# Optimization experiments

Hardware: AMD Instinct MI355X
Metric: run time of the kernel (lower is better)

The kernel has to match this reference:

```python
import jax, jax.numpy as jnp
import numpy as np

# Mamba2 hyperparams (mamba_ssm defaults given __init__ args)
D_MODEL = 512
FF = 2048
D_STATE = 128
D_CONV = 4
EXPAND = 2
D_INNER = EXPAND * D_MODEL          # 1024
HEADDIM = 64
NHEADS = D_INNER // HEADDIM         # 16
NGROUPS = 1
CONV_DIM = D_INNER + 2 * NGROUPS * D_STATE       # 1280
D_IN_PROJ = 2 * D_INNER + 2 * NGROUPS * D_STATE + NHEADS  # 2320
CHUNK = 128
EPS = 1e-5


def setup_inputs() -> dict:
    key = jax.random.key(0)
    ks = jax.random.split(key, 16)
    B, S = 8, 2048
    s = 0.02
    dt_init = jax.random.uniform(ks[4], (NHEADS,), minval=0.001, maxval=0.1)
    return {
        # forward args (dropout treated as eval / identity)
        "tgt": jax.random.normal(ks[0], (B, S, D_MODEL), jnp.float32),
        "memory": jax.random.normal(ks[1], (B, 256, D_MODEL), jnp.float32),
        "spatial_shapes": jnp.array([[16, 16]], jnp.int32),
        "level_start_index": jnp.array([0], jnp.int32),
        "valid_ratios": jnp.ones((B, 1, 2), jnp.float32),
        # Mamba2 params
        "in_proj_w": jax.random.normal(ks[2], (D_IN_PROJ, D_MODEL), jnp.float32) * s,
        "conv_w": jax.random.normal(ks[3], (CONV_DIM, D_CONV), jnp.float32) * s,
        "conv_b": jnp.zeros((CONV_DIM,), jnp.float32),
        "dt_bias": jnp.log(jnp.expm1(dt_init)),  # inverse softplus of dt_init
        "A_log": jnp.log(jax.random.uniform(ks[5], (NHEADS,), minval=1.0, maxval=16.0)),
        "D_head": jnp.ones((NHEADS,), jnp.float32),
        "norm_w": jnp.ones((D_INNER,), jnp.float32),
        "out_proj_w": jax.random.normal(ks[6], (D_MODEL, D_INNER), jnp.float32) * s,
        # LayerNorms + FFN
        "norm1_w": jnp.ones((D_MODEL,)), "norm1_b": jnp.zeros((D_MODEL,)),
        "w1": jax.random.normal(ks[7], (FF, D_MODEL), jnp.float32) * s,
        "b1": jnp.zeros((FF,)),
        "w2": jax.random.normal(ks[8], (D_MODEL, FF), jnp.float32) * s,
        "b2": jnp.zeros((D_MODEL,)),
        "norm3_w": jnp.ones((D_MODEL,)), "norm3_b": jnp.zeros((D_MODEL,)),
    }


def _layer_norm(x, w, b):
    m = jnp.mean(x, -1, keepdims=True)
    v = jnp.mean((x - m) ** 2, -1, keepdims=True)
    return (x - m) * jax.lax.rsqrt(v + EPS) * w + b


def _ssd(x, dt, A, Bm, Cm):
    # chunked selective-scan (SSD). x:(b,s,h,p) dt:(b,s,h) A:(h,) Bm,Cm:(b,s,n)
    b, s, h, p = x.shape
    n = Bm.shape[-1]
    c, l = s // CHUNK, CHUNK
    x = x.reshape(b, c, l, h, p)
    dt = dt.reshape(b, c, l, h)
    Bm = Bm.reshape(b, c, l, n)
    Cm = Cm.reshape(b, c, l, n)
    a_cs = jnp.cumsum(dt * A, axis=2)                 # (b,c,l,h) cumulative log-decay
    ac = a_cs.transpose(0, 1, 3, 2)                   # (b,c,h,l)
    mask = jnp.tril(jnp.ones((l, l), bool))
    Lmat = jnp.exp(jnp.where(mask, ac[..., :, None] - ac[..., None, :], -jnp.inf))
    # intra-chunk (causal) contribution
    Y_diag = jnp.einsum('bcin,bcjn,bchij,bcjh,bcjhp->bcihp', Cm, Bm, Lmat, dt, x)
    # per-chunk final states
    decay_end = jnp.exp(a_cs[:, :, -1:, :] - a_cs)    # (b,c,l,h)
    states = jnp.einsum('bcln,bclh,bclh,bclhp->bchpn', Bm, decay_end, dt, x)
    chunk_decay = jnp.exp(a_cs[:, :, -1, :])          # (b,c,h)
    def step(h0, inp):
        cd, st = inp
        return cd[:, :, None, None] * h0 + st, h0
    h_init = jnp.zeros((b, h, p, n), x.dtype)
    _, prev = jax.lax.scan(step, h_init,
                           (chunk_decay.transpose(1, 0, 2),
                            states.transpose(1, 0, 2, 3, 4)))
    prev = prev.transpose(1, 0, 2, 3, 4)              # (b,c,h,p,n) state at chunk start
    Y_off = jnp.einsum('bcln,bchpn,bclh->bclhp', Cm, prev, jnp.exp(a_cs))
    return (Y_diag + Y_off).reshape(b, s, h, p)


def _mamba2(u, in_proj_w, conv_w, conv_b, dt_bias, A_log, D_head, norm_w, out_proj_w):
    Bb, S, _ = u.shape
    zxbcdt = u @ in_proj_w.T                          # (b,s,2320)
    z, xBC, dt = jnp.split(zxbcdt, [D_INNER, D_INNER + CONV_DIM], axis=-1)
    # causal depthwise conv1d + silu
    xp = jnp.pad(xBC, ((0, 0), (D_CONV - 1, 0), (0, 0)))
    conv = sum(xp[:, k:k + S, :] * conv_w[:, k] for k in range(D_CONV)) + conv_b
    xBC = jax.nn.silu(conv)
    x, Bm, Cm = jnp.split(xBC, [D_INNER, D_INNER + NGROUPS * D_STATE], axis=-1)
    dt = jax.nn.softplus(dt + dt_bias)                # (b,s,h)
    A = -jnp.exp(A_log)                               # (h,)
    x = x.reshape(Bb, S, NHEADS, HEADDIM)
    y = _ssd(x, dt, A, Bm, Cm) + D_head[None, None, :, None] * x
    y = y.reshape(Bb, S, D_INNER)
    # gated RMSNorm: rmsnorm(y * silu(z)) * w
    y = y * jax.nn.silu(z)
    y = y * jax.lax.rsqrt(jnp.mean(y * y, -1, keepdims=True) + EPS) * norm_w
    return y @ out_proj_w.T


def reference(tgt, memory, spatial_shapes, level_start_index, valid_ratios,
              in_proj_w, conv_w, conv_b, dt_bias, A_log, D_head, norm_w, out_proj_w,
              norm1_w, norm1_b, w1, b1, w2, b2, norm3_w, norm3_b):
    t2 = _mamba2(tgt, in_proj_w, conv_w, conv_b, dt_bias, A_log, D_head, norm_w, out_proj_w)
    t = _layer_norm(tgt + t2, norm1_w, norm1_b)
    ff = jax.nn.gelu(t @ w1.T + b1, approximate=False) @ w2.T + b2
    return _layer_norm(t + ff, norm3_w, norm3_b)
```

## Files before the change

kernel.cpp:

```cpp
#include <hip/hip_runtime.h>
#include <hip/hip_bf16.h>
#include <math.h>


namespace {
constexpr int BB = 8;
constexpr int S = 2048;
constexpr int DM = 512;
constexpr int DIP = 2320;
constexpr int DIPP = 2432;
constexpr int DI = 1024;
constexpr int CDIM = 1280;
constexpr int NH = 16;
constexpr int HD = 64;
constexpr int DSTATE = 128;
constexpr int CH = 128;
constexpr int NC = S / CH;
constexpr int FF = 2048;
constexpr float EPS = 1e-5f;
constexpr int LP = 132;
}

using bf16_t = __hip_bfloat16;
typedef __attribute__((ext_vector_type(8))) short short8;
typedef __attribute__((ext_vector_type(4))) float f32x4;

__device__ __forceinline__ float gelu_exact(float x) {
    return 0.5f * x * (1.0f + erff(x * 0.7071067811865476f));
}
__device__ __forceinline__ unsigned short f2bfu(float f) {
    bf16_t b = __float2bfloat16(f);
    return *(unsigned short*)&b;
}
__device__ __forceinline__ float bfu2f(unsigned short u) {
    union { unsigned int i; float f; } v; v.i = (unsigned)u << 16; return v.f;
}

__device__ __forceinline__ void block_sum2(float& a, float& b) {
    #pragma unroll
    for (int o = 32; o > 0; o >>= 1) {
        a += __shfl_down(a, o, 64);
        b += __shfl_down(b, o, 64);
    }
    __shared__ float sa[4], sb[4];
    int w = threadIdx.x >> 6;
    if ((threadIdx.x & 63) == 0) { sa[w] = a; sb[w] = b; }
    __syncthreads();
    a = sa[0] + sa[1] + sa[2] + sa[3];
    b = sb[0] + sb[1] + sb[2] + sb[3];
}

template <int BM, int BK, int ACT, bool HASBIAS, bool OUTBF>
__global__ __launch_bounds__(256)
void mfma_gemm(const bf16_t* __restrict__ A, const bf16_t* __restrict__ W,
               const float* __restrict__ bias, void* __restrict__ Cout,
               int N, int K, int lda, int ldw, int ldc,
               long batchA, long batchW, long batchC)
{
    A += (long)blockIdx.z * batchA;
    W += (long)blockIdx.z * batchW;
    constexpr int NJ = (BM == 128) ? 4 : 2;
    constexpr int KO = BK / 32;
    constexpr int QA = 256 / BM;
    constexpr int TA = (BM * BK) / 2048;
    constexpr int TW = (128 * BK) / 2048;
    __shared__ bf16_t As[2][BM * BK];
    __shared__ bf16_t Ws[2][128 * BK];
    const int tid = threadIdx.x;
    const int lane = tid & 63;
    const int wave = tid >> 6;
    const long bm = (long)blockIdx.y * BM;
    const int bn = blockIdx.x * 128;

    const int rA = tid & (BM - 1);
    const int qA = tid / BM;
    const int rW = tid & 127;
    const int qW = tid >> 7;
    const bf16_t* Ag = A + (bm + rA) * (long)lda + qA * 8;
    const bf16_t* Wg = W + ((long)bn + rW) * (long)ldw + qW * 8;
    const int laoff = (qA * BM + rA) * 8;
    const int lwoff = (qW * 128 + rW) * 8;

    const int kq = lane >> 4;
    const int lr = lane & 15;
    const int wm = (BM == 128) ? (wave & 1) * 64 : 0;
    const int wn = (BM == 128) ? (wave >> 1) * 64 : wave * 32;

    f32x4 acc[4][NJ];
    #pragma unroll
    for (int i = 0; i < 4; i++)
        #pragma unroll
        for (int j = 0; j < NJ; j++) acc[i][j] = (f32x4){0.f, 0.f, 0.f, 0.f};

    short8 ra[TA], rw[TW];
    #pragma unroll
    for (int u = 0; u < TA; u++) ra[u] = *(const short8*)(Ag + u * (QA * 8));
    #pragma unroll
    for (int u = 0; u < TW; u++) rw[u] = *(const short8*)(Wg + u * 16);
    #pragma unroll
    for (int u = 0; u < TA; u++) *(short8*)&As[0][laoff + u * (QA * BM * 8)] = ra[u];
    #pragma unroll
    for (int u = 0; u < TW; u++) *(short8*)&Ws[0][lwoff + u * 2048] = rw[u];

    const int nt = K / BK;
    for (int t = 0; t < nt; t++) {
        const int cur = t & 1, nxt = cur ^ 1;
        if (t + 1 < nt) {
            const long ko = (long)(t + 1) * BK;
            #pragma unroll
            for (int u = 0; u < TA; u++) ra[u] = *(const short8*)(Ag + ko + u * (QA * 8));
            #pragma unroll
            for (int u = 0; u < TW; u++) rw[u] = *(const short8*)(Wg + ko + u * 16);
        }
        __syncthreads();
        #pragma unroll
        for (int hk = 0; hk < KO; hk++) {
            short8 af[4], bfr[NJ];
            #pragma unroll
            for (int i = 0; i < 4; i++)
                af[i] = *(const short8*)&As[cur][((hk * 4 + kq) * BM + wm + i * 16 + lr) * 8];
            #pragma unroll
            for (int j = 0; j < NJ; j++)
                bfr[j] = *(const short8*)&Ws[cur][((hk * 4 + kq) * 128 + wn + j * 16 + lr) * 8];
            #pragma unroll
            for (int i = 0; i < 4; i++)
                #pragma unroll
                for (int j = 0; j < NJ; j++)
                    acc[i][j] = __builtin_amdgcn_mfma_f32_16x16x32_bf16(af[i], bfr[j], acc[i][j], 0, 0, 0);
        }
        if (t + 1 < nt) {
            #pragma unroll
            for (int u = 0; u < TA; u++) *(short8*)&As[nxt][laoff + u * (QA * BM * 8)] = ra[u];
            #pragma unroll
            for (int u = 0; u < TW; u++) *(short8*)&Ws[nxt][lwoff + u * 2048] = rw[u];
        }
    }

    #pragma unroll
    for (int i = 0; i < 4; i++) {
        #pragma unroll
        for (int j = 0; j < NJ; j++) {
            int col = bn + wn + j * 16 + lr;
            if (col < N) {
                float bv = HASBIAS ? bias[col] : 0.f;
                #pragma unroll
                for (int r = 0; r < 4; r++) {
                    long row = bm + wm + i * 16 + kq * 4 + r;
                    float v = acc[i][j][r] + bv;
                    if (ACT == 1) v = gelu_exact(v);
                    if (OUTBF) ((bf16_t*)Cout)[row * (long)ldc + col + blockIdx.z * batchC] = __float2bfloat16(v);
                    else       ((float*)Cout)[row * (long)ldc + col + blockIdx.z * batchC] = v;
                }
            }
        }
    }
}

__global__ __launch_bounds__(256)
void dt_cvt(const float* __restrict__ tgt, const float* __restrict__ Wdt,
            const float* __restrict__ dt_bias, bf16_t* __restrict__ tgt_bf,
            float* __restrict__ dts)
{
    const int lane = threadIdx.x & 63;
    const int wave = threadIdx.x >> 6;
    float Wl[16][8];
    #pragma unroll
    for (int h = 0; h < 16; h++) {
        float4 a = *(const float4*)&Wdt[h * 512 + lane * 8];
        float4 b = *(const float4*)&Wdt[h * 512 + lane * 8 + 4];
        Wl[h][0] = a.x; Wl[h][1] = a.y; Wl[h][2] = a.z; Wl[h][3] = a.w;
        Wl[h][4] = b.x; Wl[h][5] = b.y; Wl[h][6] = b.z; Wl[h][7] = b.w;
    }
    float bs[16];
    #pragma unroll
    for (int h = 0; h < 16; h++) bs[h] = dt_bias[h];

    const long row0 = ((long)blockIdx.x * 4 + wave) * 4;
    #pragma unroll
    for (int rr = 0; rr < 4; rr++) {
        const long t = row0 + rr;
        float4 xa = *(const float4*)&tgt[t * 512 + lane * 8];
        float4 xb = *(const float4*)&tgt[t * 512 + lane * 8 + 4];
        float x[8] = {xa.x, xa.y, xa.z, xa.w, xb.x, xb.y, xb.z, xb.w};
        short8 ob;
        #pragma unroll
        for (int q = 0; q < 8; q++) ob[q] = (short)f2bfu(x[q]);
        *(short8*)&tgt_bf[t * 512 + lane * 8] = ob;

        float acc[16];
        #pragma unroll
        for (int h = 0; h < 16; h++) {
            float s = 0.f;
            #pragma unroll
            for (int q = 0; q < 8; q++) s += x[q] * Wl[h][q];
            acc[h] = s;
        }
        #pragma unroll
        for (int off = 32; off > 0; off >>= 1)
            #pragma unroll
            for (int h = 0; h < 16; h++)
                acc[h] += __shfl_xor(acc[h], off, 64);
        if (lane == 0) {
            #pragma unroll
            for (int h = 0; h < 16; h++) {
                float v = acc[h] + bs[h];
                dts[t * NH + h] = (v > 20.f) ? v : log1pf(__expf(v));
            }
        }
    }
}

__global__ __launch_bounds__(256)
void cvt_bf16(const float* __restrict__ s, bf16_t* __restrict__ d, long n)
{
    long i = ((long)blockIdx.x * 256 + threadIdx.x) * 4;
    if (i >= n) return;
    float4 v = *(const float4*)(s + i);
    d[i + 0] = __float2bfloat16(v.x);
    d[i + 1] = __float2bfloat16(v.y);
    d[i + 2] = __float2bfloat16(v.z);
    d[i + 3] = __float2bfloat16(v.w);
}

__global__ __launch_bounds__(256)
void cvt_bf16_pad(const float* __restrict__ s, bf16_t* __restrict__ d,
                  int rows_src, long total, int cols)
{
    long i = (long)blockIdx.x * 256 + threadIdx.x;
    if (i >= total) return;
    long r = i / cols;
    d[i] = __float2bfloat16(r < rows_src ? s[i] : 0.f);
}

__global__ __launch_bounds__(256)
void conv_silu_t16(const bf16_t* __restrict__ zx, const float* __restrict__ cw,
                   const float* __restrict__ cb, bf16_t* __restrict__ xBC)
{
    const int quad = blockIdx.x * 64 + (threadIdx.x & 63);
    const int wv = threadIdx.x >> 6;
    const int c = quad * 4;
    const int s0 = blockIdx.y * 64 + wv * 16;
    const long t0 = (long)blockIdx.z * S + s0;

    float wgt[4][4];
    #pragma unroll
    for (int cc = 0; cc < 4; cc++)
        #pragma unroll
        for (int k = 0; k < 4; k++) wgt[cc][k] = cw[(c + cc) * 4 + k];
    float bias[4];
    #pragma unroll
    for (int cc = 0; cc < 4; cc++) bias[cc] = cb[c + cc];

    unsigned long long rows[19];
    #pragma unroll
    for (int i = 0; i < 19; i++) {
        int s = s0 + i - 3;
        rows[i] = (s >= 0) ? *(const unsigned long long*)&zx[(t0 + i - 3) * DIP + DI + c] : 0ULL;
    }
    #pragma unroll
    for (int i = 0; i < 16; i++) {
        float v[4];
        #pragma unroll
        for (int cc = 0; cc < 4; cc++) v[cc] = bias[cc];
        #pragma unroll
        for (int k = 0; k < 4; k++) {
            unsigned long long u = rows[i + k];
            v[0] += bfu2f((unsigned short)(u      )) * wgt[0][k];
            v[1] += bfu2f((unsigned short)(u >> 16)) * wgt[1][k];
            v[2] += bfu2f((unsigned short)(u >> 32)) * wgt[2][k];
            v[3] += bfu2f((unsigned short)(u >> 48)) * wgt[3][k];
        }
        unsigned long long o = 0;
        #pragma unroll
        for (int cc = 0; cc < 4; cc++) {
            float sv = v[cc] / (1.f + __expf(-v[cc]));
            o |= (unsigned long long)f2bfu(sv) << (16 * cc);
        }
        *(unsigned long long*)&xBC[(t0 + i) * (long)CDIM + c] = o;
    }
}

__global__ __launch_bounds__(256)
void ssd_states(const bf16_t* __restrict__ xBC, const float* __restrict__ dts,
                const float* __restrict__ A_log,
                float* __restrict__ st, float* __restrict__ acs_all,
                float* __restrict__ cdlog)
{
    const int bid = blockIdx.x;
    const int nh = bid & 1;
    const int h = (bid >> 1) & 15;
    const int c = (bid >> 5) & 15;
    const int b = bid >> 9;
    const int sbid = (b * NC + c) * NH + h;
    const int tid = threadIdx.x;
    const int lane = tid & 63;
    const int wave = tid >> 6;
    __shared__ float dtv[128];
    __shared__ float acs[128];
    __shared__ float wj[128];
    __shared__ bf16_t XT[64 * LP];
    __shared__ bf16_t BwT[64 * LP];
    const long t0 = (long)b * S + (long)c * CH;
    const float Ah = -__expf(A_log[h]);

    if (tid < 128) {
        float d = dts[(t0 + tid) * NH + h];
        dtv[tid] = d;
        acs[tid] = d * Ah;
    }
    __syncthreads();
    for (int off = 1; off < 128; off <<= 1) {
        float add = 0.f;
        if (tid < 128 && tid >= off) add = acs[tid - off];
        __syncthreads();
        if (tid < 128 && tid >= off) acs[tid] += add;
        __syncthreads();
    }
    const float el = acs[127];
    if (tid < 128) wj[tid] = __expf(el - acs[tid]) * dtv[tid];
    if (nh == 0) {
        if (tid < 128) acs_all[(long)sbid * 128 + tid] = acs[tid];
        if (tid == 0) cdlog[sbid] = el;
    }
    __syncthreads();

    const int n0b = nh * 64;
    for (int i = tid; i < 4096; i += 256) {
        int p = i & 63, jp = (i >> 6) << 1;
        unsigned short a = *(const unsigned short*)&xBC[(t0 + jp) * CDIM + h * HD + p];
        unsigned short bb = *(const unsigned short*)&xBC[(t0 + jp + 1) * CDIM + h * HD + p];
        *(unsigned int*)&XT[p * LP + jp] = (unsigned)a | ((unsigned)bb << 16);
    }
    for (int i = tid; i < 4096; i += 256) {
        int n = i & 63, jp = (i >> 6) << 1;
        float v0 = __bfloat162float(xBC[(t0 + jp) * CDIM + DI + n0b + n]) * wj[jp];
        float v1 = __bfloat162float(xBC[(t0 + jp + 1) * CDIM + DI + n0b + n]) * wj[jp + 1];
        *(unsigned int*)&BwT[n * LP + jp] = (unsigned)f2bfu(v0) | ((unsigned)f2bfu(v1) << 16);
    }
    __syncthreads();

    const int kq = lane >> 4;
    const int lr = lane & 15;
    const int p0w = (wave & 1) * 32;
    const int n0w = (wave >> 1) * 32;
    f32x4 acc[2][2];
    #pragma unroll
    for (int i = 0; i < 2; i++)
        #pragma unroll
        for (int j = 0; j < 2; j++) acc[i][j] = (f32x4){0.f, 0.f, 0.f, 0.f};
    #pragma unroll
    for (int t = 0; t < 4; t++) {
        short8 af[2], bfr[2];
        #pragma unroll
        for (int i = 0; i < 2; i++)
            af[i] = *(const short8*)&XT[(p0w + i * 16 + lr) * LP + t * 32 + kq * 8];
        #pragma unroll
        for (int j = 0; j < 2; j++)
            bfr[j] = *(const short8*)&BwT[(n0w + j * 16 + lr) * LP + t * 32 + kq * 8];
        #pragma unroll
        for (int i = 0; i < 2; i++)
            #pragma unroll
            for (int j = 0; j < 2; j++)
                acc[i][j] = __builtin_amdgcn_mfma_f32_16x16x32_bf16(af[i], bfr[j], acc[i][j], 0, 0, 0);
    }
    long base = (long)sbid * 8192;
    #pragma unroll
    for (int i = 0; i < 2; i++)
        #pragma unroll
        for (int j = 0; j < 2; j++) {
            int col = n0b + n0w + j * 16 + lr;
            #pragma unroll
            for (int r = 0; r < 4; r++) {
                int p = p0w + i * 16 + kq * 4 + r;
                st[base + p * 128 + col] = acc[i][j][r];
            }
        }
}

__global__ __launch_bounds__(256)
void ssd_scan(const float* __restrict__ st, const float* __restrict__ cdlog,
              bf16_t* __restrict__ prevb)
{
    const int h = blockIdx.x & 15;
    const int b = blockIdx.x >> 4;
    const int q0 = blockIdx.y * 8;
    const int tid = threadIdx.x;
    float prev[8];
    #pragma unroll
    for (int q = 0; q < 8; q++) prev[q] = 0.f;
    for (int c = 0; c < NC; c++) {
        int bc = (b * NC + c) * NH + h;
        float cd = __expf(cdlog[bc]);
        long base = (long)bc * 8192 + (long)q0 * 256;
        #pragma unroll
        for (int q = 0; q < 8; q++) {
            long idx = base + (long)q * 256 + tid;
            float v = st[idx];
            prevb[idx] = __float2bfloat16(prev[q]);
            prev[q] = cd * prev[q] + v;
        }
    }
}

__global__ __launch_bounds__(256)
void ssd_out(const bf16_t* __restrict__ xBC, const float* __restrict__ dts,
             const bf16_t* __restrict__ G, const bf16_t* __restrict__ prevb,
             const float* __restrict__ acs_all, const float* __restrict__ D_head,
             bf16_t* __restrict__ y)
{
    const int bid = blockIdx.x;
    const int ih = bid & 1;
    const int h = (bid >> 1) & 15;
    const int c = (bid >> 5) & 15;
    const int b = bid >> 9;
    const int sbid = (b * NC + c) * NH + h;
    const int tid = threadIdx.x;
    const int lane = tid & 63;
    const int wave = tid >> 6;
    __shared__ float dtv[128];
    __shared__ float acs[128];
    __shared__ float eacs[64];
    __shared__ bf16_t Abuf[64 * LP];
    __shared__ bf16_t Bbuf[64 * LP];
    const long t0 = (long)b * S + (long)c * CH;
    const int m0b = ih * 64;

    if (tid < 128) {
        dtv[tid] = dts[(t0 + tid) * NH + h];
        acs[tid] = acs_all[(long)sbid * 128 + tid];
    }
    __syncthreads();
    if (tid < 64) eacs[tid] = __expf(acs[m0b + tid]);

    const bf16_t* Gb = G + (long)(b * NC + c) * 128 * 128;
    for (int i = tid; i < 4096; i += 256) {
        int rl = i >> 6, kp = (i & 63) << 1;
        int grow = m0b + rl;
        unsigned int g2 = *(const unsigned int*)&Gb[grow * 128 + kp];
        float w0 = (kp     <= grow) ? bfu2f((unsigned short)(g2      )) * __expf(acs[grow] - acs[kp    ]) * dtv[kp    ] : 0.f;
        float w1 = (kp + 1 <= grow) ? bfu2f((unsigned short)(g2 >> 16)) * __expf(acs[grow] - acs[kp + 1]) * dtv[kp + 1] : 0.f;
        *(unsigned int*)&Abuf[rl * LP + kp] = (unsigned)f2bfu(w0) | ((unsigned)f2bfu(w1) << 16);
    }
    for (int i = tid; i < 4096; i += 256) {
        int p = i & 63, jp = (i >> 6) << 1;
        unsigned short a = *(const unsigned short*)&xBC[(t0 + jp) * CDIM + h * HD + p];
        unsigned short bb = *(const unsigned short*)&xBC[(t0 + jp + 1) * CDIM + h * HD + p];
        *(unsigned int*)&Bbuf[p * LP + jp] = (unsigned)a | ((unsigned)bb << 16);
    }
    __syncthreads();

    const int kq = lane >> 4;
    const int lr = lane & 15;
    const int m0w = (wave & 1) * 32;
    const int p0 = (wave >> 1) * 32;
    f32x4 acc[2][2];
    #pragma unroll
    for (int i = 0; i < 2; i++)
        #pragma unroll
        for (int j = 0; j < 2; j++) acc[i][j] = (f32x4){0.f, 0.f, 0.f, 0.f};

    #pragma unroll
    for (int t = 0; t < 4; t++) {
        short8 af[2], bfr[2];
        #pragma unroll
        for (int i = 0; i < 2; i++)
            af[i] = *(const short8*)&Abuf[(m0w + i * 16 + lr) * LP + t * 32 + kq * 8];
        #pragma unroll
        for (int j = 0; j < 2; j++)
            bfr[j] = *(const short8*)&Bbuf[(p0 + j * 16 + lr) * LP + t * 32 + kq * 8];
        #pragma unroll
        for (int i = 0; i < 2; i++)
            #pragma unroll
            for (int j = 0; j < 2; j++)
                acc[i][j] = __builtin_amdgcn_mfma_f32_16x16x32_bf16(af[i], bfr[j], acc[i][j], 0, 0, 0);
    }
    const float Dh = D_head[h];
    float dx[2][2][4];
    #pragma unroll
    for (int i = 0; i < 2; i++)
        #pragma unroll
        for (int j = 0; j < 2; j++) {
            int col = p0 + j * 16 + lr;
            #pragma unroll
            for (int r = 0; r < 4; r++) {
                int rl = m0w + i * 16 + kq * 4 + r;
                dx[i][j][r] = Dh * __bfloat162float(Bbuf[col * LP + m0b + rl]);
            }
        }
    __syncthreads();

    for (int i = tid; i < 4096; i += 256) {
        int rl = i >> 6, np = (i & 63) << 1;
        unsigned int c2 = *(const unsigned int*)&xBC[(t0 + m0b + rl) * CDIM + DI + DSTATE + np];
        float e = eacs[rl];
        float v0 = e * bfu2f((unsigned short)(c2      ));
        float v1 = e * bfu2f((unsigned short)(c2 >> 16));
        *(unsigned int*)&Abuf[rl * LP + np] = (unsigned)f2bfu(v0) | ((unsigned)f2bfu(v1) << 16);
    }
    for (int i = tid; i < 4096; i += 256) {
        int p = i >> 6, np = (i & 63) << 1;
        *(unsigned int*)&Bbuf[p * LP + np] =
            *(const unsigned int*)&prevb[(long)sbid * 8192 + p * 128 + np];
    }
    __syncthreads();

    #pragma unroll
    for (int t = 0; t < 4; t++) {
        short8 af[2], bfr[2];
        #pragma unroll
        for (int i = 0; i < 2; i++)
            af[i] = *(const short8*)&Abuf[(m0w + i * 16 + lr) * LP + t * 32 + kq * 8];
        #pragma unroll
        for (int j = 0; j < 2; j++)
            bfr[j] = *(const short8*)&Bbuf[(p0 + j * 16 + lr) * LP + t * 32 + kq * 8];
        #pragma unroll
        for (int i = 0; i < 2; i++)
            #pragma unroll
            for (int j = 0; j < 2; j++)
                acc[i][j] = __builtin_amdgcn_mfma_f32_16x16x32_bf16(af[i], bfr[j], acc[i][j], 0, 0, 0);
    }

    #pragma unroll
    for (int i = 0; i < 2; i++)
        #pragma unroll
        for (int j = 0; j < 2; j++) {
            int col = p0 + j * 16 + lr;
            #pragma unroll
            for (int r = 0; r < 4; r++) {
                int rl = m0w + i * 16 + kq * 4 + r;
                y[(t0 + m0b + rl) * DI + h * HD + col] = __float2bfloat16(acc[i][j][r] + dx[i][j][r]);
            }
        }
}

__global__ __launch_bounds__(256)
void gated_rms(const bf16_t* __restrict__ y, const bf16_t* __restrict__ zx,
               const float* __restrict__ norm_w, bf16_t* __restrict__ yn)
{
    const long t = blockIdx.x;
    const int d = threadIdx.x * 4;
    unsigned long long zu = *(const unsigned long long*)&zx[t * DIP + d];
    unsigned long long yu = *(const unsigned long long*)&y[t * DI + d];
    float g[4];
    float ss = 0.f, dummy = 0.f;
    #pragma unroll
    for (int q = 0; q < 4; q++) {
        float zv = bfu2f((unsigned short)(zu >> (16 * q)));
        float yv = bfu2f((unsigned short)(yu >> (16 * q)));
        float gv = yv * (zv / (1.f + __expf(-zv)));
        g[q] = gv;
        ss += gv * gv;
    }
    block_sum2(ss, dummy);
    float scale = rsqrtf(ss * (1.f / DI) + EPS);
    unsigned long long o = 0;
    #pragma unroll
    for (int q = 0; q < 4; q++)
        o |= (unsigned long long)f2bfu(g[q] * scale * norm_w[d + q]) << (16 * q);
    *(unsigned long long*)&yn[t * DI + d] = o;
}

template <bool W16>
__global__ __launch_bounds__(256)
void add_ln(const float* __restrict__ x, const float* __restrict__ r,
            const float* __restrict__ w, const float* __restrict__ bpar,
            float* __restrict__ o32, bf16_t* __restrict__ o16)
{
    const int tid = threadIdx.x;
    const long t = blockIdx.x * 2 + (tid >> 7);
    const int i = (tid & 127) * 4;
    float4 xv = *(const float4*)(x + t * DM + i);
    float4 rv = *(const float4*)(r + t * DM + i);
    float v[4] = {xv.x + rv.x, xv.y + rv.y, xv.z + rv.z, xv.w + rv.w};
    float s = v[0] + v[1] + v[2] + v[3];
    float s2 = v[0]*v[0] + v[1]*v[1] + v[2]*v[2] + v[3]*v[3];
    #pragma unroll
    for (int o = 32; o > 0; o >>= 1) {
        s += __shfl_down(s, o, 64);
        s2 += __shfl_down(s2, o, 64);
    }
    __shared__ float sa[4], sb[4];
    int wv = tid >> 6;
    if ((tid & 63) == 0) { sa[wv] = s; sb[wv] = s2; }
    __syncthreads();
    int base = (tid >> 7) * 2;
    s = sa[base] + sa[base + 1];
    s2 = sb[base] + sb[base + 1];
    float mean = s * (1.f / DM);
    float var = s2 * (1.f / DM) - mean * mean;
    float inv = rsqrtf(var + EPS);
    float4 ov;
    float* op = (float*)&ov;
    unsigned long long o16u = 0;
    #pragma unroll
    for (int q = 0; q < 4; q++) {
        float o = (v[q] - mean) * inv * w[i + q] + bpar[i + q];
        op[q] = o;
        if (W16) o16u |= (unsigned long long)f2bfu(o) << (16 * q);
    }
    *(float4*)(o32 + t * DM + i) = ov;
    if (W16) *(unsigned long long*)&o16[t * DM + i] = o16u;
}


extern "C" void kernel_launch(void* const* d_in, const int* in_sizes, int n_in,
                              void* d_out, int out_size, void* d_ws, size_t ws_size,
                              hipStream_t stream)
{
    const float* tgt       = (const float*)d_in[0];
    const float* in_proj_w = (const float*)d_in[5];
    const float* conv_w    = (const float*)d_in[6];
    const float* conv_b    = (const float*)d_in[7];
    const float* dt_bias   = (const float*)d_in[8];
    const float* A_log     = (const float*)d_in[9];
    const float* D_head    = (const float*)d_in[10];
    const float* norm_w    = (const float*)d_in[11];
    const float* out_proj_w= (const float*)d_in[12];
    const float* norm1_w   = (const float*)d_in[13];
    const float* norm1_b   = (const float*)d_in[14];
    const float* w1        = (const float*)d_in[15];
    const float* b1        = (const float*)d_in[16];
    const float* w2        = (const float*)d_in[17];
    const float* b2        = (const float*)d_in[18];
    const float* norm3_w   = (const float*)d_in[19];
    const float* norm3_b   = (const float*)d_in[20];
    float* out = (float*)d_out;

    float* ws = (float*)d_ws;

    const size_t SZ_INW  = (size_t)DIPP * DM / 2;
    const size_t SZ_OUTW = (size_t)DM * DI / 2;
    const size_t SZ_W1   = (size_t)FF * DM / 2;
    const size_t SZ_W2   = (size_t)DM * FF / 2;
    size_t wo = 0;
    bf16_t* inW  = (bf16_t*)(ws + wo); wo += SZ_INW;
    bf16_t* outW = (bf16_t*)(ws + wo); wo += SZ_OUTW;
    bf16_t* w1b  = (bf16_t*)(ws + wo); wo += SZ_W1;
    bf16_t* w2b  = (bf16_t*)(ws + wo); wo += SZ_W2;
    const size_t WB = wo;

    const size_t PB = (size_t)S * DM / 2
                    + (size_t)S * DIP / 2
                    + (size_t)S * NH
                    + (size_t)S * CDIM / 2
                    + (size_t)NC * 128 * 128 / 2
                    + (size_t)NC * NH * 128
                    + (size_t)NC * NH
                    + (size_t)S * DI
                    + (size_t)S * DI;
    int NB = 0;
    for (int nb = 8; nb >= 1; nb >>= 1) {
        if (ws_size >= (WB + (size_t)nb * PB) * sizeof(float)) { NB = nb; break; }
    }
    if (NB == 0) return;

    {
        long n = (long)DIPP * DM;
        cvt_bf16_pad<<<(n + 255) / 256, 256, 0, stream>>>(in_proj_w, inW, DIP, n, DM);
        n = (long)DM * DI;
        cvt_bf16<<<(n / 4 + 255) / 256, 256, 0, stream>>>(out_proj_w, outW, n);
        n = (long)FF * DM;
        cvt_bf16<<<(n / 4 + 255) / 256, 256, 0, stream>>>(w1, w1b, n);
        n = (long)DM * FF;
        cvt_bf16<<<(n / 4 + 255) / 256, 256, 0, stream>>>(w2, w2b, n);
    }

    for (int b0 = 0; b0 < BB; b0 += NB) {
        const long Tg = (long)NB * S;
        size_t o = WB;
        bf16_t* tgt_bf = (bf16_t*)(ws + o); o += (size_t)Tg * DM / 2;
        bf16_t* zx     = (bf16_t*)(ws + o); o += (size_t)Tg * DIP / 2;
        float*  dts    = ws + o;            o += (size_t)Tg * NH;
        bf16_t* xBC    = (bf16_t*)(ws + o); o += (size_t)Tg * CDIM / 2;
        bf16_t* Gbuf   = (bf16_t*)(ws + o); o += (size_t)NB * NC * 128 * 128 / 2;
        float*  acs    = ws + o;            o += (size_t)NB * NC * NH * 128;
        float*  cdl    = ws + o;            o += (size_t)NB * NC * NH;
        float*  ybuf   = ws + o;            o += (size_t)Tg * DI;
        float*  st     = ws + o;            o += (size_t)Tg * DI;

        bf16_t* ybf   = (bf16_t*)ybuf;
        bf16_t* prevb = (bf16_t*)(ybuf + (size_t)Tg * DI / 2);
        bf16_t* yn  = (bf16_t*)st;
        float*  t2  = ybuf;
        float*  tb  = (float*)zx;
        bf16_t* tbb = (bf16_t*)(((float*)zx) + Tg * DM);
        bf16_t* h1  = (bf16_t*)ybuf;
        float*  fb  = (float*)xBC;

        const float* tgt_g = tgt + (long)b0 * S * DM;
        float* out_g = out + (long)b0 * S * DM;

        dt_cvt<<<Tg / 16, 256, 0, stream>>>(
            tgt_g, in_proj_w + (long)(DI + CDIM) * DM, dt_bias, tgt_bf, dts);
        mfma_gemm<128, 32, 0, false, true><<<dim3(DIPP / 128, Tg / 128, 1), 256, 0, stream>>>(
            tgt_bf, inW, nullptr, zx, DIP, DM, DM, DM, DIP, 0, 0, 0);
        conv_silu_t16<<<dim3(CDIM / 256, S / 64, NB), 256, 0, stream>>>(zx, conv_w, conv_b, xBC);
        mfma_gemm<128, 32, 0, false, true><<<dim3(1, 1, NB * NC), 256, 0, stream>>>(
            xBC + DI + DSTATE, xBC + DI, nullptr, Gbuf,
            128, DSTATE, CDIM, CDIM, 128,
            (long)CH * CDIM, (long)CH * CDIM, (long)128 * 128);
        ssd_states<<<NB * NC * NH * 2, 256, 0, stream>>>(xBC, dts, A_log, st, acs, cdl);
        ssd_scan<<<dim3(NB * NH, 4), 256, 0, stream>>>(st, cdl, prevb);
        ssd_out<<<NB * NC * NH * 2, 256, 0, stream>>>(xBC, dts, Gbuf, prevb, acs, D_head, ybf);
        gated_rms<<<Tg, 256, 0, stream>>>(ybf, zx, norm_w, yn);
        mfma_gemm<128, 64, 0, false, false><<<dim3(DM / 128, Tg / 128, 1), 256, 0, stream>>>(
            yn, outW, nullptr, t2, DM, DI, DI, DI, DM, 0, 0, 0);
        add_ln<true><<<Tg / 2, 256, 0, stream>>>(tgt_g, t2, norm1_w, norm1_b, tb, tbb);
        mfma_gemm<128, 32, 1, true, true><<<dim3(FF / 128, Tg / 128, 1), 256, 0, stream>>>(
            tbb, w1b, b1, h1, FF, DM, DM, DM, FF, 0, 0, 0);
        mfma_gemm<128, 64, 0, true, false><<<dim3(DM / 128, Tg / 128, 1), 256, 0, stream>>>(
            h1, w2b, b2, fb, DM, FF, FF, FF, DM, 0, 0, 0);
        add_ln<false><<<Tg / 2, 256, 0, stream>>>(tb, fb, norm3_w, norm3_b, out_g, nullptr);
    }
}
```

Before: 795.0 us.

## Split-K the narrow output GEMMs and remap workgroup IDs for XCD locality

The out_proj and FFN down-projection GEMMs have only N=512 output columns, which gives few workgroups. Each is now split along K into two partial GEMMs, written to separate buffers and summed inside add_ln, which gets a second residual input. The GEMM kernel also remaps workgroup IDs in strides of 8 so neighbouring tiles land on the same XCD and share L2. The split doubles the fp32 partial-output traffic and adds a launch for the FFN GEMM, and it also changes BK from 64 to 32.

```diff
diff --git a/kernel.cpp b/kernel.cpp
--- a/kernel.cpp
+++ b/kernel.cpp
@@ -69,8 +69,17 @@
     const int tid = threadIdx.x;
     const int lane = tid & 63;
     const int wave = tid >> 6;
-    const long bm = (long)blockIdx.y * BM;
-    const int bn = blockIdx.x * 128;
+
+    const int nwg = gridDim.x * gridDim.y;
+    int wgid = blockIdx.y * gridDim.x + blockIdx.x;
+    if ((nwg & 7) == 0) {
+        const int q = nwg >> 3;
+        wgid = (wgid & 7) * q + (wgid >> 3);
+    }
+    const int bxi = wgid % gridDim.x;
+    const int byi = wgid / gridDim.x;
+    const long bm = (long)byi * BM;
+    const int bn = bxi * 128;
 
     const int rA = tid & (BM - 1);
     const int qA = tid / BM;
@@ -560,10 +569,11 @@
     *(unsigned long long*)&yn[t * DI + d] = o;
 }
 
-template <bool W16>
+template <bool W16, bool R2>
 __global__ __launch_bounds__(256)
 void add_ln(const float* __restrict__ x, const float* __restrict__ r,
-            const float* __restrict__ w, const float* __restrict__ bpar,
+            const float* __restrict__ r2, const float* __restrict__ w,
+            const float* __restrict__ bpar,
             float* __restrict__ o32, bf16_t* __restrict__ o16)
 {
     const int tid = threadIdx.x;
@@ -572,6 +582,10 @@
     float4 xv = *(const float4*)(x + t * DM + i);
     float4 rv = *(const float4*)(r + t * DM + i);
     float v[4] = {xv.x + rv.x, xv.y + rv.y, xv.z + rv.z, xv.w + rv.w};
+    if (R2) {
+        float4 r2v = *(const float4*)(r2 + t * DM + i);
+        v[0] += r2v.x; v[1] += r2v.y; v[2] += r2v.z; v[3] += r2v.w;
+    }
     float s = v[0] + v[1] + v[2] + v[3];
     float s2 = v[0]*v[0] + v[1]*v[1] + v[2]*v[2] + v[3]*v[3];
     #pragma unroll
@@ -681,11 +695,13 @@
         bf16_t* ybf   = (bf16_t*)ybuf;
         bf16_t* prevb = (bf16_t*)(ybuf + (size_t)Tg * DI / 2);
         bf16_t* yn  = (bf16_t*)st;
-        float*  t2  = ybuf;
+        float*  t2a = ybuf;
+        float*  t2b = ybuf + (size_t)Tg * DM;
         float*  tb  = (float*)zx;
         bf16_t* tbb = (bf16_t*)(((float*)zx) + Tg * DM);
         bf16_t* h1  = (bf16_t*)ybuf;
-        float*  fb  = (float*)xBC;
+        float*  fb1 = (float*)xBC;
+        float*  fb2 = st;
 
         const float* tgt_g = tgt + (long)b0 * S * DM;
         float* out_g = out + (long)b0 * S * DM;
@@ -703,13 +719,18 @@
         ssd_scan<<<dim3(NB * NH, 4), 256, 0, stream>>>(st, cdl, prevb);
         ssd_out<<<NB * NC * NH * 2, 256, 0, stream>>>(xBC, dts, Gbuf, prevb, acs, D_head, ybf);
         gated_rms<<<Tg, 256, 0, stream>>>(ybf, zx, norm_w, yn);
-        mfma_gemm<128, 64, 0, false, false><<<dim3(DM / 128, Tg / 128, 1), 256, 0, stream>>>(
-            yn, outW, nullptr, t2, DM, DI, DI, DI, DM, 0, 0, 0);
-        add_ln<true><<<Tg / 2, 256, 0, stream>>>(tgt_g, t2, norm1_w, norm1_b, tb, tbb);
+        mfma_gemm<128, 32, 0, false, false><<<dim3(DM / 128, Tg / 128, 2), 256, 0, stream>>>(
+            yn, outW, nullptr, t2a, DM, DI / 2, DI, DI, DM,
+            (long)(DI / 2), (long)(DI / 2), (long)Tg * DM);
+        add_ln<true, true><<<Tg / 2, 256, 0, stream>>>(
+            tgt_g, t2a, t2b, norm1_w, norm1_b, tb, tbb);
         mfma_gemm<128, 32, 1, true, true><<<dim3(FF / 128, Tg / 128, 1), 256, 0, stream>>>(
             tbb, w1b, b1, h1, FF, DM, DM, DM, FF, 0, 0, 0);
-        mfma_gemm<128, 64, 0, true, false><<<dim3(DM / 128, Tg / 128, 1), 256, 0, stream>>>(
-            h1, w2b, b2, fb, DM, FF, FF, FF, DM, 0, 0, 0);
-        add_ln<false><<<Tg / 2, 256, 0, stream>>>(tb, fb, norm3_w, norm3_b, out_g, nullptr);
-    }
-}
+        mfma_gemm<128, 32, 0, false, false><<<dim3(DM / 128, Tg / 128, 1), 256, 0, stream>>>(
+            h1, w2b, nullptr, fb1, DM, FF / 2, FF, FF, DM, 0, 0, 0);
+        mfma_gemm<128, 32, 0, true, false><<<dim3(DM / 128, Tg / 128, 1), 256, 0, stream>>>(
+            h1 + FF / 2, w2b + FF / 2, b2, fb2, DM, FF / 2, FF, FF, DM, 0, 0, 0);
+        add_ln<false, true><<<Tg / 2, 256, 0, stream>>>(
+            tb, fb1, fb2, norm3_w, norm3_b, out_g, nullptr);
+    }
+}
```

Result: slower. 817.3 us (+2.8%).
